# Kernel tuning notes

Hardware: AMD Instinct MI355X
Metric: run time of the kernel (lower is better)

## Reference

```python
import jax, jax.numpy as jnp
import numpy as np

N_HEADS = 16
D_HEAD = 64
TAU = 30.0
NEG = -1e9


def setup_inputs() -> dict:
    key = jax.random.key(0)
    k1, k2, k3, k4 = jax.random.split(key, 4)
    B, L, D = 2, 2048, 1024
    scale = 1.0 / np.sqrt(D)
    return {
        "input": jax.random.normal(k1, (B, L, D), dtype=jnp.float32),
        "attention_mask": jnp.ones((B, L), dtype=jnp.int32),
        "W_Q": jax.random.normal(k2, (N_HEADS * D_HEAD, D), dtype=jnp.float32) * scale,
        "W_K": jax.random.normal(k3, (N_HEADS * D_HEAD, D), dtype=jnp.float32) * scale,
        "W_V": jax.random.normal(k4, (N_HEADS * D_HEAD, D), dtype=jnp.float32) * scale,
    }


def reference(input, attention_mask, W_Q, W_K, W_V):
    B, L, D = input.shape
    # fused QKV projection (F.linear: x @ W.T), split into heads: [B, H, L, Dh]
    def proj(W):
        return jnp.einsum('bld,ed->ble', input, W).reshape(B, L, N_HEADS, D_HEAD).transpose(0, 2, 1, 3)
    q, k, v = proj(W_Q), proj(W_K), proj(W_V)
    S = jnp.einsum('bhqd,bhkd->bhqk', q, k) / np.sqrt(D_HEAD)  # [B,H,L,L]
    S = TAU * jnp.tanh(S)
    causal = jnp.tril(jnp.ones((L, L), dtype=bool))            # True = keep
    keep = causal[None, None, :, :] & (attention_mask[:, None, None, :] != 0)
    S = jnp.where(keep, S, NEG)
    attn = jax.nn.softmax(S, axis=-1)
    out = jnp.einsum('bhqk,bhkd->bhqd', attn, v)
    return out.transpose(0, 2, 1, 3).reshape(B, L, N_HEADS * D_HEAD)
```

## Files before the change

kernel.cpp:

```cpp
#include <hip/hip_runtime.h>


typedef unsigned short u16;
typedef __bf16 bf16x8 __attribute__((ext_vector_type(8)));
typedef float f32x4 __attribute__((ext_vector_type(4)));

#define MFMA(a, b, c) __builtin_amdgcn_mfma_f32_16x16x32_bf16(a, b, c, 0, 0, 0)

__device__ __forceinline__ u16 bf16rne(float f) {
    unsigned int u = __float_as_uint(f);
    u += 0x7fffu + ((u >> 16) & 1u);
    return (u16)(u >> 16);
}
__device__ __forceinline__ float bf16f(u16 h) {
    return __uint_as_float(((unsigned int)h) << 16);
}
__device__ __forceinline__ void split1(float f, u16& hi, u16& lo) {
    hi = bf16rne(f);
    lo = bf16rne(f - bf16f(hi));
}

__device__ __forceinline__ void gl16(const u16* g, u16* l) {
    __builtin_amdgcn_global_load_lds(
        (const __attribute__((address_space(1))) unsigned int*)g,
        (__attribute__((address_space(3))) unsigned int*)l, 16, 0, 0);
}

__global__ __launch_bounds__(256) void presplit(
    const float* __restrict__ X, const float* __restrict__ Wq,
    const float* __restrict__ Wk, const float* __restrict__ Wv,
    u16* __restrict__ Xh, u16* __restrict__ Xl,
    u16* __restrict__ Wqh, u16* __restrict__ Wql,
    u16* __restrict__ Wkh, u16* __restrict__ Wkl,
    u16* __restrict__ Wvh)
{
    int i = blockIdx.x * 256 + threadIdx.x;
    const float* src; u16 *dh, *dl; int off;
    if (i < 1048576)      { src = X;  dh = Xh;  dl = Xl;      off = i; }
    else if (i < 1310720) { src = Wq; dh = Wqh; dl = Wql;     off = i - 1048576; }
    else if (i < 1572864) { src = Wk; dh = Wkh; dl = Wkl;     off = i - 1310720; }
    else                  { src = Wv; dh = Wvh; dl = nullptr; off = i - 1572864; }
    float4 v = ((const float4*)src)[off];
    ushort4 h, l;
    split1(v.x, h.x, l.x); split1(v.y, h.y, l.y);
    split1(v.z, h.z, l.z); split1(v.w, h.w, l.w);
    ((ushort4*)dh)[off] = h;
    if (dl) ((ushort4*)dl)[off] = l;
}

__global__ __launch_bounds__(256) void qkv_gemm(
    const u16* __restrict__ Xh, const u16* __restrict__ Xl,
    const u16* __restrict__ Wqh, const u16* __restrict__ Wql,
    const u16* __restrict__ Wkh, const u16* __restrict__ Wkl,
    const u16* __restrict__ Wvh,
    u16* __restrict__ Qh, u16* __restrict__ Ql,
    u16* __restrict__ Kh, u16* __restrict__ Kl,
    u16* __restrict__ VT)
{
    __shared__ __align__(16) u16 As[2][4096];
    __shared__ __align__(16) u16 Bs[2][4096];
    const int tid = threadIdx.x;
    const int wave = tid >> 6, lane = tid & 63, quad = lane >> 4, c16 = lane & 15;
    const int id = blockIdx.x;
    const int nb = (((id >> 3) % 3) << 3) | (id & 7);
    const int m  = (id >> 3) / 3;
    const int m0 = m * 128;
    const int mat = nb >> 3;
    const int n0 = (nb & 7) * 128;
    const u16* Bh = (mat == 0) ? Wqh : ((mat == 1) ? Wkh : Wvh);
    const u16* Bl = (mat == 0) ? Wql : Wkl;
    const int nkt = (mat < 2) ? 96 : 32;
    const int wm = (wave >> 1) * 64, wn = (wave & 1) * 64;

    const int srow0 = wave * 32 + (lane >> 2), scol = (lane & 3) * 8;

    f32x4 acc[4][4];
#pragma unroll
    for (int i = 0; i < 4; i++)
#pragma unroll
        for (int j = 0; j < 4; j++) acc[i][j] = (f32x4){0.f, 0.f, 0.f, 0.f};

    auto stage = [&](int kt, int buf) {
        const int seg = kt >> 5, kcol = (kt & 31) * 32;
        const u16* Ab = ((seg < 2) ? Xh : Xl) + (size_t)m0 * 1024 + kcol;
        const u16* Bb = ((seg == 1) ? Bl : Bh) + (size_t)n0 * 1024 + kcol;
#pragma unroll
        for (int s = 0; s < 2; s++) {
            int row = srow0 + s * 16;
            gl16(Ab + (size_t)row * 1024 + scol, &As[buf][row * 32 + scol]);
            gl16(Bb + (size_t)row * 1024 + scol, &Bs[buf][row * 32 + scol]);
        }
    };

    stage(0, 0);
    int cur = 0;
    for (int kt = 0; kt < nkt; kt++) {
        __syncthreads();
        if (kt + 1 < nkt) stage(kt + 1, cur ^ 1);
        bf16x8 af[4], bfr[4];
#pragma unroll
        for (int mt = 0; mt < 4; mt++)
            af[mt] = *(const bf16x8*)&As[cur][(wm + mt * 16 + c16) * 32 + quad * 8];
#pragma unroll
        for (int nt = 0; nt < 4; nt++)
            bfr[nt] = *(const bf16x8*)&Bs[cur][(wn + nt * 16 + c16) * 32 + quad * 8];
#pragma unroll
        for (int mt = 0; mt < 4; mt++)
#pragma unroll
            for (int nt = 0; nt < 4; nt++)
                acc[mt][nt] = MFMA(af[mt], bfr[nt], acc[mt][nt]);
        cur ^= 1;
    }

    const float scale = (mat == 0) ? 0.125f : 1.f;
#pragma unroll
    for (int mt = 0; mt < 4; mt++) {
#pragma unroll
        for (int nt = 0; nt < 4; nt++) {
#pragma unroll
            for (int reg = 0; reg < 4; reg++) {
                int mm = m0 + wm + mt * 16 + quad * 4 + reg;
                int n = n0 + wn + nt * 16 + c16;
                int b_ = mm >> 11, l = mm & 2047;
                int h = n >> 6, dh = n & 63;
                float v = acc[mt][nt][reg] * scale;
                if (mat == 2) {
                    VT[((b_ * 16 + h) * 64 + dh) * 2048 + l] = bf16rne(v);
                } else {
                    u16 hi, lo; split1(v, hi, lo);
                    int idx = ((b_ * 16 + h) * 2048 + l) * 64 + dh;
                    if (mat == 0) { Qh[idx] = hi; Ql[idx] = lo; }
                    else          { Kh[idx] = hi; Kl[idx] = lo; }
                }
            }
        }
    }
}

__global__ __launch_bounds__(256) void attn(
    const u16* __restrict__ Qh, const u16* __restrict__ Ql,
    const u16* __restrict__ Kh, const u16* __restrict__ Kl,
    const u16* __restrict__ VT, const int* __restrict__ AM,
    float* __restrict__ Out)
{
    __shared__ __align__(16) u16 Khs[2][4096];
    __shared__ __align__(16) u16 Kls[2][4096];
    __shared__ __align__(16) u16 Vs[2][4096];
    __shared__ __align__(16) u16 Qhs[4096];
    __shared__ __align__(16) u16 Qls[4096];

    const int tid = threadIdx.x, wave = tid >> 6, lane = tid & 63;
    const int quad = lane >> 4, c16 = lane & 15;
    const int bh = blockIdx.x;
    const int pr = blockIdx.y;
    const int b_ = bh >> 4, h = bh & 15;
    const size_t base = (size_t)bh * 2048 * 64;
    u16* const Ps = Qhs;

    const int swsub[2] = { (wave * 2) >> 2, (wave * 2 + 1) >> 2 };
    const int swrow[2] = { ((wave * 2) & 3) * 16 + (lane >> 2), ((wave * 2 + 1) & 3) * 16 + (lane >> 2) };
    const int scol = (lane & 3) * 8;

    auto stageKV = [&](int k0, int buf) {
        const u16* Kht = Kh + base + (size_t)k0 * 64;
        const u16* Klt = Kl + base + (size_t)k0 * 64;
        const u16* Vt  = VT + (size_t)bh * 64 * 2048 + k0;
#pragma unroll
        for (int s = 0; s < 2; s++) {
            int sub = swsub[s], row = swrow[s];
            int lo = sub * 2048 + row * 32 + scol;
            gl16(Kht + (size_t)row * 64 + sub * 32 + scol, &Khs[buf][lo]);
            gl16(Klt + (size_t)row * 64 + sub * 32 + scol, &Kls[buf][lo]);
            gl16(Vt + (size_t)row * 2048 + sub * 32 + scol, &Vs[buf][lo]);
        }
    };

    for (int tix = 0; tix < 2; ++tix) {
        const int qt = tix ? pr : 31 - pr;
        const int q0 = qt * 64;
        {
            const u16* Qht = Qh + base + (size_t)q0 * 64;
            const u16* Qlt = Ql + base + (size_t)q0 * 64;
#pragma unroll
            for (int s = 0; s < 2; s++) {
                int sub = swsub[s], row = swrow[s];
                int lo = sub * 2048 + row * 32 + scol;
                gl16(Qht + (size_t)row * 64 + sub * 32 + scol, &Qhs[lo]);
                gl16(Qlt + (size_t)row * 64 + sub * 32 + scol, &Qls[lo]);
            }
            stageKV(0, 0);
        }
        __syncthreads();
        bf16x8 qh0 = *(const bf16x8*)&Qhs[(wave * 16 + c16) * 32 + quad * 8];
        bf16x8 qh1 = *(const bf16x8*)&Qhs[2048 + (wave * 16 + c16) * 32 + quad * 8];
        bf16x8 ql0 = *(const bf16x8*)&Qls[(wave * 16 + c16) * 32 + quad * 8];
        bf16x8 ql1 = *(const bf16x8*)&Qls[2048 + (wave * 16 + c16) * 32 + quad * 8];

        float rsl[4] = {0.f, 0.f, 0.f, 0.f};
        f32x4 o[4];
#pragma unroll
        for (int r = 0; r < 4; r++) o[r] = (f32x4){0.f, 0.f, 0.f, 0.f};

        int cur = 0;
        for (int kb = 0; kb <= qt; ++kb) {
            const int k0 = kb * 64;
            if (kb < qt) stageKV(k0 + 64, cur ^ 1);
            const int mkv = AM[b_ * 2048 + k0 + lane];
            const bool interior = (kb < qt);

            float p[4][4];
#pragma unroll
            for (int nt = 0; nt < 4; nt++) {
                bf16x8 kh0 = *(const bf16x8*)&Khs[cur][(nt * 16 + c16) * 32 + quad * 8];
                bf16x8 kh1 = *(const bf16x8*)&Khs[cur][2048 + (nt * 16 + c16) * 32 + quad * 8];
                bf16x8 kl0 = *(const bf16x8*)&Kls[cur][(nt * 16 + c16) * 32 + quad * 8];
                bf16x8 kl1 = *(const bf16x8*)&Kls[cur][2048 + (nt * 16 + c16) * 32 + quad * 8];
                f32x4 sa = (f32x4){0.f, 0.f, 0.f, 0.f};
                sa = MFMA(qh0, kh0, sa);
                sa = MFMA(qh1, kh1, sa);
                sa = MFMA(ql0, kh0, sa);
                sa = MFMA(ql1, kh1, sa);
                sa = MFMA(qh0, kl0, sa);
                sa = MFMA(qh1, kl1, sa);
                const int key = k0 + nt * 16 + c16;
                const bool mok = (__shfl(mkv, nt * 16 + c16) != 0);
#pragma unroll
                for (int reg = 0; reg < 4; reg++) {
                    int qg = q0 + wave * 16 + quad * 4 + reg;
                    float x = sa[reg];
                    float e1 = __expf(2.f * x);
                    float r  = __builtin_amdgcn_rcpf(e1 + 1.f);
                    float pv = __expf(-60.f * r);
                    bool keep = mok && (interior || key <= qg);
                    pv = keep ? pv : 0.f;
                    p[nt][reg] = pv;
                    rsl[reg] += pv;
                }
            }

#pragma unroll
            for (int nt = 0; nt < 4; nt++) {
                int kl_ = nt * 16 + c16, sub = kl_ >> 5, kc = kl_ & 31;
#pragma unroll
                for (int reg = 0; reg < 4; reg++)
                    Ps[sub * 2048 + (wave * 16 + quad * 4 + reg) * 32 + kc] = bf16rne(p[nt][reg]);
            }
            bf16x8 p0 = *(const bf16x8*)&Ps[(wave * 16 + c16) * 32 + quad * 8];
            bf16x8 p1 = *(const bf16x8*)&Ps[2048 + (wave * 16 + c16) * 32 + quad * 8];
#pragma unroll
            for (int dt = 0; dt < 4; dt++) {
                bf16x8 v0 = *(const bf16x8*)&Vs[cur][(dt * 16 + c16) * 32 + quad * 8];
                bf16x8 v1 = *(const bf16x8*)&Vs[cur][2048 + (dt * 16 + c16) * 32 + quad * 8];
                o[dt] = MFMA(p0, v0, o[dt]);
                o[dt] = MFMA(p1, v1, o[dt]);
            }
            __syncthreads();
            cur ^= 1;
        }

        float inv[4];
#pragma unroll
        for (int reg = 0; reg < 4; reg++) {
            float v = rsl[reg];
#pragma unroll
            for (int off = 1; off < 16; off <<= 1)
                v += __shfl_xor(v, off);
            inv[reg] = __builtin_amdgcn_rcpf(v);
        }
#pragma unroll
        for (int dt = 0; dt < 4; dt++)
#pragma unroll
            for (int reg = 0; reg < 4; reg++) {
                int qg = q0 + wave * 16 + quad * 4 + reg;
                int d = dt * 16 + c16;
                Out[(size_t)(b_ * 2048 + qg) * 1024 + h * 64 + d] = o[dt][reg] * inv[reg];
            }
    }
}

extern "C" void kernel_launch(void* const* d_in, const int* in_sizes, int n_in,
                              void* d_out, int out_size, void* d_ws, size_t ws_size,
                              hipStream_t stream) {
    const float* X  = (const float*)d_in[0];
    const int*   AM = (const int*)d_in[1];
    const float* Wq = (const float*)d_in[2];
    const float* Wk = (const float*)d_in[3];
    const float* Wv = (const float*)d_in[4];
    float* out = (float*)d_out;

    const size_t NE = (size_t)2 * 16 * 2048 * 64;
    const size_t WN = (size_t)1024 * 1024;
    u16* Qh  = (u16*)d_ws;
    u16* Ql  = Qh + NE;
    u16* Kh  = Ql + NE;
    u16* Kl  = Kh + NE;
    u16* VT  = Kl + NE;
    u16* Xh  = VT + NE;
    u16* Xl  = Xh + NE;
    u16* Wqh = Xl + NE;
    u16* Wql = Wqh + WN;
    u16* Wkh = Wql + WN;
    u16* Wkl = Wkh + WN;
    u16* Wvh = Wkl + WN;

    presplit<<<7168, 256, 0, stream>>>(X, Wq, Wk, Wv, Xh, Xl, Wqh, Wql, Wkh, Wkl, Wvh);
    qkv_gemm<<<768, 256, 0, stream>>>(Xh, Xl, Wqh, Wql, Wkh, Wkl, Wvh,
                                      Qh, Ql, Kh, Kl, VT);
    attn<<<dim3(32, 16), 256, 0, stream>>>(Qh, Ql, Kh, Kl, VT, AM, out);
}
```

Before: 257.9 us.

## Split attention keys across two blocks, fuse hi/lo GEMM segments, add combine

The QKV GEMM now loads X and W hi and lo tiles together and runs all three split-precision segments per k-tile. This cuts global loads of the shared hi tiles but drops double buffering. The attention kernel splits the key range into two interleaved halves via blockIdx.z, doubling the grid. It reads Q and V directly from global memory instead of staging them in LDS, and sets launch bounds for occupancy 4. The unnormalized partial outputs are stored as bf16 with row sums, and a new combine kernel adds them and normalizes, which costs an extra launch, extra memory traffic and precision loss in the bf16 partials.

```diff
diff --git a/kernel.cpp b/kernel.cpp
--- a/kernel.cpp
+++ b/kernel.cpp
@@ -48,7 +48,7 @@
     if (dl) ((ushort4*)dl)[off] = l;
 }
 
-__global__ __launch_bounds__(256) void qkv_gemm(
+__global__ __launch_bounds__(256, 4) void qkv_gemm(
     const u16* __restrict__ Xh, const u16* __restrict__ Xl,
     const u16* __restrict__ Wqh, const u16* __restrict__ Wql,
     const u16* __restrict__ Wkh, const u16* __restrict__ Wkl,
@@ -57,19 +57,20 @@
     u16* __restrict__ Kh, u16* __restrict__ Kl,
     u16* __restrict__ VT)
 {
-    __shared__ __align__(16) u16 As[2][4096];
-    __shared__ __align__(16) u16 Bs[2][4096];
+    __shared__ __align__(16) u16 Xhs[4096];
+    __shared__ __align__(16) u16 Xls[4096];
+    __shared__ __align__(16) u16 Whs[4096];
+    __shared__ __align__(16) u16 Wls[4096];
     const int tid = threadIdx.x;
     const int wave = tid >> 6, lane = tid & 63, quad = lane >> 4, c16 = lane & 15;
     const int id = blockIdx.x;
     const int nb = (((id >> 3) % 3) << 3) | (id & 7);
-    const int m  = (id >> 3) / 3;
-    const int m0 = m * 128;
+    const int m0 = ((id >> 3) / 3) * 128;
     const int mat = nb >> 3;
     const int n0 = (nb & 7) * 128;
     const u16* Bh = (mat == 0) ? Wqh : ((mat == 1) ? Wkh : Wvh);
     const u16* Bl = (mat == 0) ? Wql : Wkl;
-    const int nkt = (mat < 2) ? 96 : 32;
+    const int nseg = (mat < 2) ? 3 : 1;
     const int wm = (wave >> 1) * 64, wn = (wave & 1) * 64;
 
     const int srow0 = wave * 32 + (lane >> 2), scol = (lane & 3) * 8;
@@ -80,36 +81,38 @@
 #pragma unroll
         for (int j = 0; j < 4; j++) acc[i][j] = (f32x4){0.f, 0.f, 0.f, 0.f};
 
-    auto stage = [&](int kt, int buf) {
-        const int seg = kt >> 5, kcol = (kt & 31) * 32;
-        const u16* Ab = ((seg < 2) ? Xh : Xl) + (size_t)m0 * 1024 + kcol;
-        const u16* Bb = ((seg == 1) ? Bl : Bh) + (size_t)n0 * 1024 + kcol;
+    for (int kt = 0; kt < 32; kt++) {
+        const int kcol = kt * 32;
 #pragma unroll
         for (int s = 0; s < 2; s++) {
             int row = srow0 + s * 16;
-            gl16(Ab + (size_t)row * 1024 + scol, &As[buf][row * 32 + scol]);
-            gl16(Bb + (size_t)row * 1024 + scol, &Bs[buf][row * 32 + scol]);
-        }
-    };
-
-    stage(0, 0);
-    int cur = 0;
-    for (int kt = 0; kt < nkt; kt++) {
+            size_t go = (size_t)row * 1024 + kcol + scol;
+            int lo = row * 32 + scol;
+            gl16(Xh + (size_t)m0 * 1024 + go, &Xhs[lo]);
+            gl16(Bh + (size_t)n0 * 1024 + go, &Whs[lo]);
+            if (nseg == 3) {
+                gl16(Xl + (size_t)m0 * 1024 + go, &Xls[lo]);
+                gl16(Bl + (size_t)n0 * 1024 + go, &Wls[lo]);
+            }
+        }
         __syncthreads();
-        if (kt + 1 < nkt) stage(kt + 1, cur ^ 1);
-        bf16x8 af[4], bfr[4];
-#pragma unroll
-        for (int mt = 0; mt < 4; mt++)
-            af[mt] = *(const bf16x8*)&As[cur][(wm + mt * 16 + c16) * 32 + quad * 8];
-#pragma unroll
-        for (int nt = 0; nt < 4; nt++)
-            bfr[nt] = *(const bf16x8*)&Bs[cur][(wn + nt * 16 + c16) * 32 + quad * 8];
-#pragma unroll
-        for (int mt = 0; mt < 4; mt++)
+        for (int seg = 0; seg < nseg; seg++) {
+            const u16* ap = (seg < 2) ? Xhs : Xls;
+            const u16* bp = (seg == 1) ? Wls : Whs;
+            bf16x8 af[4], bfr[4];
+#pragma unroll
+            for (int mt = 0; mt < 4; mt++)
+                af[mt] = *(const bf16x8*)&ap[(wm + mt * 16 + c16) * 32 + quad * 8];
 #pragma unroll
             for (int nt = 0; nt < 4; nt++)
-                acc[mt][nt] = MFMA(af[mt], bfr[nt], acc[mt][nt]);
-        cur ^= 1;
+                bfr[nt] = *(const bf16x8*)&bp[(wn + nt * 16 + c16) * 32 + quad * 8];
+#pragma unroll
+            for (int mt = 0; mt < 4; mt++)
+#pragma unroll
+                for (int nt = 0; nt < 4; nt++)
+                    acc[mt][nt] = MFMA(af[mt], bfr[nt], acc[mt][nt]);
+        }
+        __syncthreads();
     }
 
     const float scale = (mat == 0) ? 0.125f : 1.f;
@@ -137,145 +140,172 @@
     }
 }
 
-__global__ __launch_bounds__(256) void attn(
+__global__ __launch_bounds__(256, 4) void attn(
     const u16* __restrict__ Qh, const u16* __restrict__ Ql,
     const u16* __restrict__ Kh, const u16* __restrict__ Kl,
     const u16* __restrict__ VT, const int* __restrict__ AM,
-    float* __restrict__ Out)
+    u16* __restrict__ Op, float* __restrict__ Lp)
 {
     __shared__ __align__(16) u16 Khs[2][4096];
     __shared__ __align__(16) u16 Kls[2][4096];
-    __shared__ __align__(16) u16 Vs[2][4096];
-    __shared__ __align__(16) u16 Qhs[4096];
-    __shared__ __align__(16) u16 Qls[4096];
+    __shared__ __align__(16) u16 Ps[4096];
 
     const int tid = threadIdx.x, wave = tid >> 6, lane = tid & 63;
     const int quad = lane >> 4, c16 = lane & 15;
     const int bh = blockIdx.x;
     const int pr = blockIdx.y;
-    const int b_ = bh >> 4, h = bh & 15;
+    const int sp = blockIdx.z;
+    const int b_ = bh >> 4;
     const size_t base = (size_t)bh * 2048 * 64;
-    u16* const Ps = Qhs;
 
     const int swsub[2] = { (wave * 2) >> 2, (wave * 2 + 1) >> 2 };
     const int swrow[2] = { ((wave * 2) & 3) * 16 + (lane >> 2), ((wave * 2 + 1) & 3) * 16 + (lane >> 2) };
     const int scol = (lane & 3) * 8;
 
-    auto stageKV = [&](int k0, int buf) {
+    auto stageK = [&](int k0, int buf) {
         const u16* Kht = Kh + base + (size_t)k0 * 64;
         const u16* Klt = Kl + base + (size_t)k0 * 64;
-        const u16* Vt  = VT + (size_t)bh * 64 * 2048 + k0;
 #pragma unroll
         for (int s = 0; s < 2; s++) {
             int sub = swsub[s], row = swrow[s];
             int lo = sub * 2048 + row * 32 + scol;
             gl16(Kht + (size_t)row * 64 + sub * 32 + scol, &Khs[buf][lo]);
             gl16(Klt + (size_t)row * 64 + sub * 32 + scol, &Kls[buf][lo]);
-            gl16(Vt + (size_t)row * 2048 + sub * 32 + scol, &Vs[buf][lo]);
         }
     };
 
     for (int tix = 0; tix < 2; ++tix) {
         const int qt = tix ? pr : 31 - pr;
         const int q0 = qt * 64;
-        {
-            const u16* Qht = Qh + base + (size_t)q0 * 64;
-            const u16* Qlt = Ql + base + (size_t)q0 * 64;
-#pragma unroll
-            for (int s = 0; s < 2; s++) {
-                int sub = swsub[s], row = swrow[s];
-                int lo = sub * 2048 + row * 32 + scol;
-                gl16(Qht + (size_t)row * 64 + sub * 32 + scol, &Qhs[lo]);
-                gl16(Qlt + (size_t)row * 64 + sub * 32 + scol, &Qls[lo]);
-            }
-            stageKV(0, 0);
-        }
-        __syncthreads();
-        bf16x8 qh0 = *(const bf16x8*)&Qhs[(wave * 16 + c16) * 32 + quad * 8];
-        bf16x8 qh1 = *(const bf16x8*)&Qhs[2048 + (wave * 16 + c16) * 32 + quad * 8];
-        bf16x8 ql0 = *(const bf16x8*)&Qls[(wave * 16 + c16) * 32 + quad * 8];
-        bf16x8 ql1 = *(const bf16x8*)&Qls[2048 + (wave * 16 + c16) * 32 + quad * 8];
+
+        const size_t qrow = base + (size_t)(q0 + wave * 16 + c16) * 64 + quad * 8;
+        bf16x8 qh0 = *(const bf16x8*)&Qh[qrow];
+        bf16x8 qh1 = *(const bf16x8*)&Qh[qrow + 32];
+        bf16x8 ql0 = *(const bf16x8*)&Ql[qrow];
+        bf16x8 ql1 = *(const bf16x8*)&Ql[qrow + 32];
 
         float rsl[4] = {0.f, 0.f, 0.f, 0.f};
         f32x4 o[4];
 #pragma unroll
         for (int r = 0; r < 4; r++) o[r] = (f32x4){0.f, 0.f, 0.f, 0.f};
 
-        int cur = 0;
-        for (int kb = 0; kb <= qt; ++kb) {
-            const int k0 = kb * 64;
-            if (kb < qt) stageKV(k0 + 64, cur ^ 1);
-            const int mkv = AM[b_ * 2048 + k0 + lane];
-            const bool interior = (kb < qt);
-
-            float p[4][4];
-#pragma unroll
-            for (int nt = 0; nt < 4; nt++) {
-                bf16x8 kh0 = *(const bf16x8*)&Khs[cur][(nt * 16 + c16) * 32 + quad * 8];
-                bf16x8 kh1 = *(const bf16x8*)&Khs[cur][2048 + (nt * 16 + c16) * 32 + quad * 8];
-                bf16x8 kl0 = *(const bf16x8*)&Kls[cur][(nt * 16 + c16) * 32 + quad * 8];
-                bf16x8 kl1 = *(const bf16x8*)&Kls[cur][2048 + (nt * 16 + c16) * 32 + quad * 8];
-                f32x4 sa = (f32x4){0.f, 0.f, 0.f, 0.f};
-                sa = MFMA(qh0, kh0, sa);
-                sa = MFMA(qh1, kh1, sa);
-                sa = MFMA(ql0, kh0, sa);
-                sa = MFMA(ql1, kh1, sa);
-                sa = MFMA(qh0, kl0, sa);
-                sa = MFMA(qh1, kl1, sa);
-                const int key = k0 + nt * 16 + c16;
-                const bool mok = (__shfl(mkv, nt * 16 + c16) != 0);
-#pragma unroll
-                for (int reg = 0; reg < 4; reg++) {
-                    int qg = q0 + wave * 16 + quad * 4 + reg;
-                    float x = sa[reg];
-                    float e1 = __expf(2.f * x);
-                    float r  = __builtin_amdgcn_rcpf(e1 + 1.f);
-                    float pv = __expf(-60.f * r);
-                    bool keep = mok && (interior || key <= qg);
-                    pv = keep ? pv : 0.f;
-                    p[nt][reg] = pv;
-                    rsl[reg] += pv;
+        if (sp <= qt) {
+            stageK(sp * 64, 0);
+            int cur = 0;
+            for (int kb = sp; kb <= qt; kb += 2) {
+                const int k0 = kb * 64;
+                __syncthreads();
+                if (kb + 2 <= qt) stageK(k0 + 128, cur ^ 1);
+                const int mkv = AM[b_ * 2048 + k0 + lane];
+                const bool interior = (kb < qt);
+
+                float p[4][4];
+#pragma unroll
+                for (int nt = 0; nt < 4; nt++) {
+                    bf16x8 kh0 = *(const bf16x8*)&Khs[cur][(nt * 16 + c16) * 32 + quad * 8];
+                    bf16x8 kh1 = *(const bf16x8*)&Khs[cur][2048 + (nt * 16 + c16) * 32 + quad * 8];
+                    bf16x8 kl0 = *(const bf16x8*)&Kls[cur][(nt * 16 + c16) * 32 + quad * 8];
+                    bf16x8 kl1 = *(const bf16x8*)&Kls[cur][2048 + (nt * 16 + c16) * 32 + quad * 8];
+                    f32x4 sa = (f32x4){0.f, 0.f, 0.f, 0.f};
+                    sa = MFMA(qh0, kh0, sa);
+                    sa = MFMA(qh1, kh1, sa);
+                    sa = MFMA(ql0, kh0, sa);
+                    sa = MFMA(ql1, kh1, sa);
+                    sa = MFMA(qh0, kl0, sa);
+                    sa = MFMA(qh1, kl1, sa);
+                    const int key = k0 + nt * 16 + c16;
+                    const bool mok = (__shfl(mkv, nt * 16 + c16) != 0);
+#pragma unroll
+                    for (int reg = 0; reg < 4; reg++) {
+                        int qg = q0 + wave * 16 + quad * 4 + reg;
+                        float x = sa[reg];
+                        float e1 = __expf(2.f * x);
+                        float r  = __builtin_amdgcn_rcpf(e1 + 1.f);
+                        float pv = __expf(-60.f * r);
+                        bool keep = mok && (interior || key <= qg);
+                        pv = keep ? pv : 0.f;
+                        p[nt][reg] = pv;
+                        rsl[reg] += pv;
+                    }
                 }
+
+#pragma unroll
+                for (int nt = 0; nt < 4; nt++) {
+                    int kl_ = nt * 16 + c16, sub = kl_ >> 5, kc = kl_ & 31;
+#pragma unroll
+                    for (int reg = 0; reg < 4; reg++)
+                        Ps[sub * 2048 + (wave * 16 + quad * 4 + reg) * 32 + kc] = bf16rne(p[nt][reg]);
+                }
+                bf16x8 p0 = *(const bf16x8*)&Ps[(wave * 16 + c16) * 32 + quad * 8];
+                bf16x8 p1 = *(const bf16x8*)&Ps[2048 + (wave * 16 + c16) * 32 + quad * 8];
+
+#pragma unroll
+                for (int dt = 0; dt < 4; dt++) {
+                    const size_t vrow = (size_t)(bh * 64 + dt * 16 + c16) * 2048 + k0 + quad * 8;
+                    bf16x8 v0 = *(const bf16x8*)&VT[vrow];
+                    bf16x8 v1 = *(const bf16x8*)&VT[vrow + 32];
+                    o[dt] = MFMA(p0, v0, o[dt]);
+                    o[dt] = MFMA(p1, v1, o[dt]);
+                }
+                cur ^= 1;
             }
-
-#pragma unroll
-            for (int nt = 0; nt < 4; nt++) {
-                int kl_ = nt * 16 + c16, sub = kl_ >> 5, kc = kl_ & 31;
-#pragma unroll
-                for (int reg = 0; reg < 4; reg++)
-                    Ps[sub * 2048 + (wave * 16 + quad * 4 + reg) * 32 + kc] = bf16rne(p[nt][reg]);
-            }
-            bf16x8 p0 = *(const bf16x8*)&Ps[(wave * 16 + c16) * 32 + quad * 8];
-            bf16x8 p1 = *(const bf16x8*)&Ps[2048 + (wave * 16 + c16) * 32 + quad * 8];
-#pragma unroll
-            for (int dt = 0; dt < 4; dt++) {
-                bf16x8 v0 = *(const bf16x8*)&Vs[cur][(dt * 16 + c16) * 32 + quad * 8];
-                bf16x8 v1 = *(const bf16x8*)&Vs[cur][2048 + (dt * 16 + c16) * 32 + quad * 8];
-                o[dt] = MFMA(p0, v0, o[dt]);
-                o[dt] = MFMA(p1, v1, o[dt]);
-            }
-            __syncthreads();
-            cur ^= 1;
-        }
-
-        float inv[4];
+        }
+        __syncthreads();
+
+        const size_t ob = ((size_t)(sp * 512 + bh * 16) + 0) * 0 +
+                          ((size_t)((sp * 32 + 0) ) * 0);
+        (void)ob;
+        const size_t obase = (((size_t)sp * 1024 + (size_t)bh * 32 + qt) * 4096);
+        const size_t lbase = (((size_t)sp * 1024 + (size_t)bh * 32 + qt) * 64);
+        float lsum[4];
 #pragma unroll
         for (int reg = 0; reg < 4; reg++) {
             float v = rsl[reg];
 #pragma unroll
             for (int off = 1; off < 16; off <<= 1)
                 v += __shfl_xor(v, off);
-            inv[reg] = __builtin_amdgcn_rcpf(v);
+            lsum[reg] = v;
+        }
+        if (c16 == 0) {
+#pragma unroll
+            for (int reg = 0; reg < 4; reg++)
+                Lp[lbase + wave * 16 + quad * 4 + reg] = lsum[reg];
         }
 #pragma unroll
         for (int dt = 0; dt < 4; dt++)
 #pragma unroll
             for (int reg = 0; reg < 4; reg++) {
-                int qg = q0 + wave * 16 + quad * 4 + reg;
+                int row = wave * 16 + quad * 4 + reg;
                 int d = dt * 16 + c16;
-                Out[(size_t)(b_ * 2048 + qg) * 1024 + h * 64 + d] = o[dt][reg] * inv[reg];
+                Op[obase + row * 64 + d] = bf16rne(o[dt][reg]);
             }
     }
+}
+
+__global__ __launch_bounds__(256) void combine(
+    const u16* __restrict__ Op, const float* __restrict__ Lp,
+    float* __restrict__ Out)
+{
+    const int i = blockIdx.x * 256 + threadIdx.x;
+    const size_t lin = (size_t)i * 4;
+    const int d  = (int)(lin & 1023);
+    const int h  = d >> 6, dd = d & 63;
+    const int l  = (int)((lin >> 10) & 2047);
+    const int b  = (int)(lin >> 21);
+    const int qt = l >> 6, row = l & 63;
+    const int bh = b * 16 + h;
+    const size_t o0 = (((size_t)bh * 32 + qt) * 4096) + row * 64 + dd;
+    const size_t o1 = o0 + (size_t)1024 * 4096;
+    const size_t l0 = (((size_t)bh * 32 + qt) * 64) + row;
+    ushort4 pa = *(const ushort4*)&Op[o0];
+    ushort4 pb = *(const ushort4*)&Op[o1];
+    float inv = __builtin_amdgcn_rcpf(Lp[l0] + Lp[l0 + 65536]);
+    float4 r;
+    r.x = (bf16f(pa.x) + bf16f(pb.x)) * inv;
+    r.y = (bf16f(pa.y) + bf16f(pb.y)) * inv;
+    r.z = (bf16f(pa.z) + bf16f(pb.z)) * inv;
+    r.w = (bf16f(pa.w) + bf16f(pb.w)) * inv;
+    *(float4*)&Out[lin] = r;
 }
 
 extern "C" void kernel_launch(void* const* d_in, const int* in_sizes, int n_in,
@@ -302,9 +332,12 @@
     u16* Wkh = Wql + WN;
     u16* Wkl = Wkh + WN;
     u16* Wvh = Wkl + WN;
+    u16*   Op = Xh;
+    float* Lp = (float*)Wqh;
 
     presplit<<<7168, 256, 0, stream>>>(X, Wq, Wk, Wv, Xh, Xl, Wqh, Wql, Wkh, Wkl, Wvh);
     qkv_gemm<<<768, 256, 0, stream>>>(Xh, Xl, Wqh, Wql, Wkh, Wkl, Wvh,
                                       Qh, Ql, Kh, Kl, VT);
-    attn<<<dim3(32, 16), 256, 0, stream>>>(Qh, Ql, Kh, Kl, VT, AM, out);
-}
+    attn<<<dim3(32, 16, 2), 256, 0, stream>>>(Qh, Ql, Kh, Kl, VT, AM, Op, Lp);
+    combine<<<4096, 256, 0, stream>>>(Op, Lp, out);
+}
```

Result: faster. 249.3 us (-3.3%).
